# Performance work log

Hardware: AMD Instinct MI355X
Metric: run time of the kernel (lower is better)

The kernel has to match this reference:

```python
import jax, jax.numpy as jnp
import numpy as np

B, H, L = 16, 256, 4096
C, KD, NS = 1, 32, 8  # channels, kernel_dim, num_scales


def _interp_linear(k, s):
    """torch F.interpolate(mode='linear', align_corners=False) with integer scale s.
    k: (C, H, Lin) -> (C, H, Lin*s)."""
    if s == 1:
        return k
    Lin = k.shape[-1]
    x = (jnp.arange(Lin * s, dtype=jnp.float32) + 0.5) / s - 0.5
    x = jnp.clip(x, 0.0, Lin - 1)
    x0 = jnp.floor(x).astype(jnp.int32)
    x1 = jnp.minimum(x0 + 1, Lin - 1)
    w = (x - x0.astype(jnp.float32)).astype(k.dtype)
    return k[..., x0] * (1.0 - w) + k[..., x1] * w


def _build_kernel(kernels):
    # multiplier = linspace(decay_min=2, decay_max=2, H) -> all 2.0, shape (1,H,1)
    multiplier = jnp.linspace(2.0, 2.0, H).reshape(1, H, 1)
    parts = []
    for i in range(NS):
        s = 2 ** max(0, i - 1)  # init_scale = 0
        parts.append(_interp_linear(kernels[i], s) * multiplier ** (NS - i - 1))
    return jnp.concatenate(parts, axis=-1)  # (C, H, 4096)


def setup_inputs() -> dict:
    key = jax.random.key(0)
    k0, k1, k2, k3, k4 = jax.random.split(key, 5)
    u = jax.random.normal(k0, (B, H, L), jnp.float32)
    kernels = jax.random.normal(k1, (NS, C, H, KD), jnp.float32)
    D = jax.random.normal(k2, (C, H), jnp.float32)
    W_out = jax.random.normal(k3, (H, C * H), jnp.float32) * 0.05
    b_out = jax.random.normal(k4, (H,), jnp.float32) * 0.05
    return {"u": u, "kernels": kernels, "D": D, "W_out": W_out, "b_out": b_out}


def reference(u, kernels, D, W_out, b_out):
    k = _build_kernel(kernels)  # (C, H, Lk)
    Lk = k.shape[-1]
    if Lk > L:
        k = k[..., :L]
    elif Lk < L:
        k = jnp.pad(k, ((0, 0), (0, 0), (0, L - Lk)))
    # kernel_norm is detached on first forward
    norm = jax.lax.stop_gradient(jnp.linalg.norm(k, axis=-1, keepdims=True))
    k = k / norm
    n = 2 * L
    k_f = jnp.fft.rfft(k, n=n)  # (C, H, L+1) complex
    u_f = jnp.fft.rfft(u, n=n)  # (B, H, L+1) complex
    y_f = jnp.einsum('bhl,chl->bchl', u_f, k_f)
    y = jnp.fft.irfft(y_f, n=n)[..., :L]  # (B, C, H, L)
    y = y + jnp.einsum('bhl,ch->bchl', u, D)
    y = y.reshape(B, C * H, L)
    y = jax.nn.gelu(y, approximate=False)  # nn.GELU exact
    y = jnp.transpose(y, (0, 2, 1))  # (B, L, C*H)
    y = y @ W_out.T + b_out  # output_linear: C*H -> H
    return jnp.transpose(y, (0, 2, 1))  # (B, H, L)
```

## Files before the change

### kernel.cpp

```cpp
#include <hip/hip_runtime.h>


#define C1f 0.92387953251128674f
#define S1f 0.38268343236508977f
#define C2f 0.70710678118654752f

typedef __attribute__((ext_vector_type(8))) short bf16x8;
typedef __attribute__((ext_vector_type(4))) float f32x4;

static __device__ __forceinline__ unsigned short f2bf(float f) {
  unsigned u = __float_as_uint(f);
  u += 0x7FFFu + ((u >> 16) & 1u);
  return (unsigned short)(u >> 16);
}

static __device__ __forceinline__ void cmul(float& ar, float& ai, float br, float bi) {
  float t = ar * br - ai * bi;
  ai = ar * bi + ai * br;
  ar = t;
}

static __device__ __forceinline__ float gelu_t(float x) {
  float x2 = x * x;
  float t = x * __builtin_fmaf(0.044715f, x2, 1.f);
  float e = __builtin_amdgcn_exp2f(-2.3022650966f * t);
  return x * __builtin_amdgcn_rcpf(1.f + e);
}

#define LGKM()                                              \
  {                                                         \
    asm volatile("s_waitcnt lgkmcnt(0)" ::: "memory");      \
    __builtin_amdgcn_sched_barrier(0);                      \
  }

__device__ __constant__ float W32C[16] = {
  1.f, 0.98078528040323044913f, 0.92387953251128675613f, 0.83146961230254523708f,
  0.70710678118654752440f, 0.55557023301960222474f, 0.38268343236508977173f,
  0.19509032201612826785f, 0.f, -0.19509032201612826785f, -0.38268343236508977173f,
  -0.55557023301960222474f, -0.70710678118654752440f, -0.83146961230254523708f,
  -0.92387953251128675613f, -0.98078528040323044913f};
__device__ __constant__ float W32S[16] = {
  0.f, 0.19509032201612826785f, 0.38268343236508977173f, 0.55557023301960222474f,
  0.70710678118654752440f, 0.83146961230254523708f, 0.92387953251128675613f,
  0.98078528040323044913f, 1.f, 0.98078528040323044913f, 0.92387953251128675613f,
  0.83146961230254523708f, 0.70710678118654752440f, 0.55557023301960222474f,
  0.38268343236508977173f, 0.19509032201612826785f};

template <bool ZH>
static __device__ __forceinline__ void dft16_fwd_t(float* xr, float* xi) {
  const float wr[8] = {1.f, C1f, C2f, S1f, 0.f, -S1f, -C2f, -C1f};
  const float wi[8] = {0.f, -S1f, -C2f, -C1f, -1.f, -C1f, -C2f, -S1f};
#pragma unroll
  for (int j = 0; j < 8; ++j) {
    if (ZH) {
      float ar = xr[j], ai = xi[j];
      xr[j + 8] = ar * wr[j] - ai * wi[j];
      xi[j + 8] = ar * wi[j] + ai * wr[j];
    } else {
      float ar = xr[j], ai = xi[j], br = xr[j + 8], bi = xi[j + 8];
      xr[j] = ar + br; xi[j] = ai + bi;
      float dr = ar - br, di = ai - bi;
      xr[j + 8] = dr * wr[j] - di * wi[j];
      xi[j + 8] = dr * wi[j] + di * wr[j];
    }
  }
#pragma unroll
  for (int h = 0; h < 2; ++h) {
#pragma unroll
    for (int j = 0; j < 4; ++j) {
      int i0 = h * 8 + j, i1 = i0 + 4;
      float ar = xr[i0], ai = xi[i0], br = xr[i1], bi = xi[i1];
      xr[i0] = ar + br; xi[i0] = ai + bi;
      float dr = ar - br, di = ai - bi;
      xr[i1] = dr * wr[2 * j] - di * wi[2 * j];
      xi[i1] = dr * wi[2 * j] + di * wr[2 * j];
    }
  }
#pragma unroll
  for (int h = 0; h < 4; ++h) {
    int base = h * 4;
    {
      int i0 = base, i1 = base + 2;
      float ar = xr[i0], ai = xi[i0], br = xr[i1], bi = xi[i1];
      xr[i0] = ar + br; xi[i0] = ai + bi;
      xr[i1] = ar - br; xi[i1] = ai - bi;
    }
    {
      int i0 = base + 1, i1 = base + 3;
      float ar = xr[i0], ai = xi[i0], br = xr[i1], bi = xi[i1];
      xr[i0] = ar + br; xi[i0] = ai + bi;
      float dr = ar - br, di = ai - bi;
      xr[i1] = di; xi[i1] = -dr;
    }
  }
#pragma unroll
  for (int h = 0; h < 8; ++h) {
    int i0 = h * 2, i1 = i0 + 1;
    float ar = xr[i0], ai = xi[i0], br = xr[i1], bi = xi[i1];
    xr[i0] = ar + br; xi[i0] = ai + bi;
    xr[i1] = ar - br; xi[i1] = ai - bi;
  }
}

template <bool HALF>
static __device__ __forceinline__ void dft16_inv_t(float* xr, float* xi) {
  const float wr[8] = {1.f, C1f, C2f, S1f, 0.f, -S1f, -C2f, -C1f};
  const float wi[8] = {0.f, S1f, C2f, C1f, 1.f, C1f, C2f, S1f};
#pragma unroll
  for (int h = 0; h < 8; ++h) {
    int i0 = h * 2, i1 = i0 + 1;
    float ar = xr[i0], ai = xi[i0], br = xr[i1], bi = xi[i1];
    xr[i0] = ar + br; xi[i0] = ai + bi;
    xr[i1] = ar - br; xi[i1] = ai - bi;
  }
#pragma unroll
  for (int h = 0; h < 4; ++h) {
    int base = h * 4;
    {
      int i0 = base, i1 = base + 2;
      float ar = xr[i0], ai = xi[i0], tr = xr[i1], ti = xi[i1];
      xr[i0] = ar + tr; xi[i0] = ai + ti;
      xr[i1] = ar - tr; xi[i1] = ai - ti;
    }
    {
      int i0 = base + 1, i1 = base + 3;
      float ar = xr[i0], ai = xi[i0], br = xr[i1], bi = xi[i1];
      float tr = -bi, ti = br;
      xr[i0] = ar + tr; xi[i0] = ai + ti;
      xr[i1] = ar - tr; xi[i1] = ai - ti;
    }
  }
#pragma unroll
  for (int h = 0; h < 2; ++h) {
#pragma unroll
    for (int j = 0; j < 4; ++j) {
      int i0 = h * 8 + j, i1 = i0 + 4;
      float br = xr[i1], bi = xi[i1];
      float tr = br * wr[2 * j] - bi * wi[2 * j];
      float ti = br * wi[2 * j] + bi * wr[2 * j];
      float ar = xr[i0], ai = xi[i0];
      xr[i0] = ar + tr; xi[i0] = ai + ti;
      xr[i1] = ar - tr; xi[i1] = ai - ti;
    }
  }
#pragma unroll
  for (int j = 0; j < 8; ++j) {
    int i0 = j, i1 = j + 8;
    float br = xr[i1], bi = xi[i1];
    float tr = br * wr[j] - bi * wi[j];
    float ti = br * wi[j] + bi * wr[j];
    float ar = xr[i0], ai = xi[i0];
    xr[i0] = ar + tr; xi[i0] = ai + ti;
    if (!HALF) { xr[i1] = ar - tr; xi[i1] = ai - ti; }
  }
}

#define REV_INIT constexpr int REV[16] = {0, 8, 4, 12, 2, 10, 6, 14, 1, 9, 5, 13, 3, 11, 7, 15}

#define TWCHAIN(XR, XI, CR, CI)                         \
  {                                                     \
    float pr_ = (CR), pi_ = (CI);                       \
    cmul(XR[8], XI[8], pr_, pi_);                       \
    _Pragma("unroll") for (int k = 2; k < 16; ++k) {    \
      cmul(pr_, pi_, (CR), (CI));                       \
      cmul(XR[REV[k]], XI[REV[k]], pr_, pi_);           \
    }                                                   \
  }

static __device__ __forceinline__ void fft8192_fwd(float* xr, float* xi, float* lbuf,
                                                   int t, const float2* __restrict__ tw) {
  REV_INIT;
  int bs1 = t + (t >> 5);
  int bg1 = ((t >> 5) << 9) + (t & 31) + ((t >> 5) << 4);
  int qq = t & 1;
  int bg2 = 33 * (t >> 1) + qq;
  dft16_fwd_t<true>(xr, xi);
  {
    float2 w1 = tw[t];
    TWCHAIN(xr, xi, w1.x, w1.y);
  }
#pragma unroll
  for (int j = 0; j < 16; ++j) lbuf[bs1 + 528 * REV[j]] = xr[j];
  __syncthreads();
#pragma unroll
  for (int m = 0; m < 16; ++m) xr[m] = lbuf[bg1 + 33 * m];
  __syncthreads();
#pragma unroll
  for (int j = 0; j < 16; ++j) lbuf[bs1 + 528 * REV[j]] = xi[j];
  __syncthreads();
#pragma unroll
  for (int m = 0; m < 16; ++m) xi[m] = lbuf[bg1 + 33 * m];
  dft16_fwd_t<false>(xr, xi);
  {
    float2 w1 = tw[(t & 31) << 4];
    TWCHAIN(xr, xi, w1.x, w1.y);
  }
  LGKM();
#pragma unroll
  for (int j = 0; j < 16; ++j) lbuf[bg1 + 33 * REV[j]] = xr[j];
  LGKM();
#pragma unroll
  for (int m = 0; m < 16; ++m) xr[m] = lbuf[bg2 + 2 * m];
  LGKM();
#pragma unroll
  for (int j = 0; j < 16; ++j) lbuf[bg1 + 33 * REV[j]] = xi[j];
  LGKM();
#pragma unroll
  for (int m = 0; m < 16; ++m) xi[m] = lbuf[bg2 + 2 * m];
  dft16_fwd_t<false>(xr, xi);
  if (qq) {
#pragma unroll
    for (int k = 1; k < 16; ++k) cmul(xr[REV[k]], xi[REV[k]], W32C[k], -W32S[k]);
  }
  float sgn = qq ? -1.f : 1.f;
#pragma unroll
  for (int j = 0; j < 16; ++j) {
    float pr = __shfl_xor(xr[j], 1);
    float pi = __shfl_xor(xi[j], 1);
    xr[j] = sgn * xr[j] + pr;
    xi[j] = sgn * xi[j] + pi;
  }
}

static __device__ __forceinline__ void fft8192_inv(float* xr, float* xi, float* lbuf,
                                                   int t, const float2* __restrict__ tw) {
  REV_INIT;
  int bs1 = t + (t >> 5);
  int bg1 = ((t >> 5) << 9) + (t & 31) + ((t >> 5) << 4);
  int qq = t & 1;
  int bg2 = 33 * (t >> 1) + qq;
  float sgn = qq ? -1.f : 1.f;
#pragma unroll
  for (int j = 0; j < 16; ++j) {
    float pr = __shfl_xor(xr[j], 1);
    float pi = __shfl_xor(xi[j], 1);
    xr[j] = sgn * xr[j] + pr;
    xi[j] = sgn * xi[j] + pi;
  }
  if (qq) {
#pragma unroll
    for (int k = 1; k < 16; ++k) cmul(xr[REV[k]], xi[REV[k]], W32C[k], W32S[k]);
  }
  dft16_inv_t<false>(xr, xi);
  LGKM();
#pragma unroll
  for (int m = 0; m < 16; ++m) lbuf[bg2 + 2 * m] = xr[m];
  LGKM();
#pragma unroll
  for (int j = 0; j < 16; ++j) xr[j] = lbuf[bg1 + 33 * REV[j]];
  LGKM();
#pragma unroll
  for (int m = 0; m < 16; ++m) lbuf[bg2 + 2 * m] = xi[m];
  LGKM();
#pragma unroll
  for (int j = 0; j < 16; ++j) xi[j] = lbuf[bg1 + 33 * REV[j]];
  {
    float2 w1 = tw[(t & 31) << 4];
    TWCHAIN(xr, xi, w1.x, -w1.y);
  }
  dft16_inv_t<false>(xr, xi);
  LGKM();
#pragma unroll
  for (int m = 0; m < 16; ++m) lbuf[bg1 + 33 * m] = xr[m];
  __syncthreads();
#pragma unroll
  for (int j = 0; j < 16; ++j) xr[j] = lbuf[bs1 + 528 * REV[j]];
  __syncthreads();
#pragma unroll
  for (int m = 0; m < 16; ++m) lbuf[bg1 + 33 * m] = xi[m];
  __syncthreads();
#pragma unroll
  for (int j = 0; j < 16; ++j) xi[j] = lbuf[bs1 + 528 * REV[j]];
  {
    float2 w1 = tw[t];
    TWCHAIN(xr, xi, w1.x, -w1.y);
  }
  dft16_inv_t<true>(xr, xi);
}

__global__ void __launch_bounds__(256) gconv_setup(
    const float* __restrict__ kernels,
    const float* __restrict__ W_out,
    float* __restrict__ k_norm,
    float2* __restrict__ tw,
    unsigned short* __restrict__ Wbf)
{
  int blk = blockIdx.x;
  int tid = threadIdx.x;
  if (blk < 256) {
    int h = blk;
    __shared__ float red[256];
    float val[16];
    float ss = 0.0f;
#pragma unroll
    for (int r = 0; r < 16; ++r) {
      int l = tid + 256 * r;
      int i;
      if (l < 32) i = 0;
      else if (l < 64) i = 1;
      else i = (31 - __clz(l)) - 4;
      int off = (i == 0) ? 0 : (16 << i);
      int s = (i <= 1) ? 1 : (1 << (i - 1));
      float mult = (float)(1 << (7 - i));
      int j = l - off;
      const float* kb = kernels + ((size_t)i * 256 + h) * 32;
      float v;
      if (s == 1) {
        v = kb[j];
      } else {
        float x = ((float)j + 0.5f) / (float)s - 0.5f;
        x = fminf(fmaxf(x, 0.0f), 31.0f);
        float xf = floorf(x);
        int x0 = (int)xf;
        int x1 = min(x0 + 1, 31);
        float w = x - xf;
        v = kb[x0] * (1.0f - w) + kb[x1] * w;
      }
      v *= mult;
      val[r] = v;
      ss += v * v;
    }
    red[tid] = ss;
    __syncthreads();
    for (int o = 128; o > 0; o >>= 1) {
      if (tid < o) red[tid] += red[tid + o];
      __syncthreads();
    }
    float inv = 1.0f / sqrtf(red[0]);
#pragma unroll
    for (int r = 0; r < 16; ++r)
      k_norm[(size_t)h * 4096 + tid + 256 * r] = val[r] * inv;
  } else if (blk < 258) {
    int idx = (blk - 256) * 256 + tid;
    double ang = -6.283185307179586477 * (double)idx / 8192.0;
    tw[idx] = make_float2((float)cos(ang), (float)sin(ang));
  } else {
    int o = (blk - 258) * 256 + tid;
    Wbf[o] = f2bf(W_out[o]);
  }
}

__global__ void __launch_bounds__(512, 4) gconv_kfft(
    const float* __restrict__ k_norm,
    const float* __restrict__ Dvec,
    const float2* __restrict__ tw,
    float2* __restrict__ Kst)
{
  __shared__ float lbuf[8448];
  int h = blockIdx.x;
  int t = threadIdx.x;
  float xr[16], xi[16];
  const float* kn = k_norm + ((size_t)h << 12);
#pragma unroll
  for (int m = 0; m < 8; ++m) { xr[m] = kn[t + (m << 9)]; xi[m] = 0.f; }
#pragma unroll
  for (int m = 8; m < 16; ++m) { xr[m] = 0.f; xi[m] = 0.f; }
  fft8192_fwd(xr, xi, lbuf, t, tw);
  float Dh = Dvec[h];
  const float sc = 1.0f / 8192.0f;
  float2* out = Kst + ((size_t)h << 13) + (t << 4);
#pragma unroll
  for (int j = 0; j < 16; ++j)
    out[j] = make_float2((xr[j] + Dh) * sc, xi[j] * sc);
}

__global__ void __launch_bounds__(512, 4) gconv_main(
    const float* __restrict__ u,
    const float2* __restrict__ tw,
    const float2* __restrict__ Kst,
    unsigned short* __restrict__ g)
{
  __shared__ float lbuf[8448];
  int blk = blockIdx.x;
  int h = blk & 255;
  int pb = blk >> 8;
  int t = threadIdx.x;
  const float* u0 = u + ((size_t)(pb * 256 + h) << 12);
  const float* u1 = u + ((size_t)((pb + 8) * 256 + h) << 12);
  float xr[16], xi[16];
#pragma unroll
  for (int m = 0; m < 8; ++m) { xr[m] = u0[t + (m << 9)]; xi[m] = u1[t + (m << 9)]; }
#pragma unroll
  for (int m = 8; m < 16; ++m) { xr[m] = 0.f; xi[m] = 0.f; }
  fft8192_fwd(xr, xi, lbuf, t, tw);
  const float2* kr = Kst + ((size_t)h << 13) + (t << 4);
#pragma unroll
  for (int j = 0; j < 16; ++j) {
    float2 kv = kr[j];
    cmul(xr[j], xi[j], kv.x, kv.y);
  }
  fft8192_inv(xr, xi, lbuf, t, tw);
  unsigned short* g0 = g + ((size_t)(pb * 256 + h) << 12) + t;
  unsigned short* g1 = g + ((size_t)((pb + 8) * 256 + h) << 12) + t;
#pragma unroll
  for (int m = 0; m < 8; ++m) {
    g0[m << 9] = f2bf(gelu_t(xr[m]));
    g1[m << 9] = f2bf(gelu_t(xi[m]));
  }
}

__global__ void __launch_bounds__(256) gconv_out(
    const unsigned short* __restrict__ g,
    const unsigned short* __restrict__ Wbf,
    const float* __restrict__ b_out,
    float* __restrict__ out)
{
  __shared__ unsigned short As[128][40];
  __shared__ unsigned short Bs[32][132];
  int l0 = blockIdx.x * 128;
  int m0 = blockIdx.y * 128;
  int b  = blockIdx.z;
  int tid = threadIdx.x;
  int lane = tid & 63, wid = tid >> 6;
  int wm = (wid >> 1) * 64, wl = (wid & 1) * 64;
  int lhi = lane >> 4, llo = lane & 15;
  f32x4 acc[4][4];
#pragma unroll
  for (int a = 0; a < 4; ++a)
#pragma unroll
    for (int c = 0; c < 4; ++c) acc[a][c] = (f32x4){0.f, 0.f, 0.f, 0.f};

  for (int ks = 0; ks < 8; ++ks) {
    int k0 = ks * 32;
#pragma unroll
    for (int i = 0; i < 2; ++i) {
      int idx = tid + i * 256;
      int m = idx >> 2, c = idx & 3;
      *(uint4*)&As[m][c * 8] =
          *(const uint4*)(Wbf + ((size_t)(m0 + m) << 8) + k0 + c * 8);
      int k = idx >> 4, cc = idx & 15;
      const unsigned short* gp =
          g + ((size_t)(b * 256 + k0 + k) << 12) + l0 + cc * 8;
      ((uint2*)&Bs[k][cc * 8])[0] = ((const uint2*)gp)[0];
      ((uint2*)&Bs[k][cc * 8])[1] = ((const uint2*)gp)[1];
    }
    __syncthreads();
    int kk = lhi * 8;
    bf16x8 af[4], bfr[4];
#pragma unroll
    for (int f = 0; f < 4; ++f)
      af[f] = *(bf16x8*)&As[wm + f * 16 + llo][kk];
#pragma unroll
    for (int f = 0; f < 4; ++f) {
      bf16x8 v;
#pragma unroll
      for (int j = 0; j < 8; ++j)
        v[j] = (short)Bs[kk + j][wl + f * 16 + llo];
      bfr[f] = v;
    }
#pragma unroll
    for (int fm = 0; fm < 4; ++fm)
#pragma unroll
      for (int fl = 0; fl < 4; ++fl)
        acc[fm][fl] = __builtin_amdgcn_mfma_f32_16x16x32_bf16(
            af[fm], bfr[fl], acc[fm][fl], 0, 0, 0);
    __syncthreads();
  }
#pragma unroll
  for (int fm = 0; fm < 4; ++fm) {
#pragma unroll
    for (int r = 0; r < 4; ++r) {
      int m = m0 + wm + fm * 16 + lhi * 4 + r;
      float bias = b_out[m];
      float* op = out + ((size_t)(b * 256 + m) << 12) + l0 + wl + llo;
#pragma unroll
      for (int fl = 0; fl < 4; ++fl)
        op[fl * 16] = acc[fm][fl][r] + bias;
    }
  }
}

extern "C" void kernel_launch(void* const* d_in, const int* in_sizes, int n_in,
                              void* d_out, int out_size, void* d_ws, size_t ws_size,
                              hipStream_t stream) {
  (void)in_sizes; (void)n_in; (void)out_size; (void)ws_size;
  const float* u       = (const float*)d_in[0];
  const float* kernels = (const float*)d_in[1];
  const float* Dvec    = (const float*)d_in[2];
  const float* W_out   = (const float*)d_in[3];
  const float* b_out   = (const float*)d_in[4];
  float* out = (float*)d_out;
  char* ws = (char*)d_ws;

  float*  k_norm = (float*)(ws);
  float2* tw     = (float2*)(ws + (4u << 20));
  unsigned short* Wbf = (unsigned short*)(ws + (4u << 20) + (128u << 10));
  float2* Kst    = (float2*)(ws + (8u << 20));
  unsigned short* g = (unsigned short*)(ws + (24u << 20));

  gconv_setup<<<514, 256, 0, stream>>>(kernels, W_out, k_norm, tw, Wbf);
  gconv_kfft<<<256, 512, 0, stream>>>(k_norm, Dvec, tw, Kst);
  gconv_main<<<2048, 512, 0, stream>>>(u, tw, Kst, g);
  dim3 gd(32, 2, 16);
  gconv_out<<<gd, 256, 0, stream>>>(g, Wbf, b_out, out);
}
```

Measured before the change: 106.7 us.

## Process two batch-pairs per block with interleaved software-pipelined FFT stages

gconv_main now handles two complex FFT pairs (four batch rows) per block and interleaves their stages, so the register-level DFT work of one pair overlaps the shared-memory transposes and barriers of the other. The grid is halved to 1024 blocks. Twiddles and the kernel-spectrum pointer are loaded once and reused for both pairs. The cost is twice the register arrays per thread, which under launch bounds (512,4) risks spills or lower occupancy.

```diff
diff --git a/kernel.cpp b/kernel.cpp
--- a/kernel.cpp
+++ b/kernel.cpp
@@ -220,62 +220,6 @@
     xr[j] = sgn * xr[j] + pr;
     xi[j] = sgn * xi[j] + pi;
   }
-}
-
-static __device__ __forceinline__ void fft8192_inv(float* xr, float* xi, float* lbuf,
-                                                   int t, const float2* __restrict__ tw) {
-  REV_INIT;
-  int bs1 = t + (t >> 5);
-  int bg1 = ((t >> 5) << 9) + (t & 31) + ((t >> 5) << 4);
-  int qq = t & 1;
-  int bg2 = 33 * (t >> 1) + qq;
-  float sgn = qq ? -1.f : 1.f;
-#pragma unroll
-  for (int j = 0; j < 16; ++j) {
-    float pr = __shfl_xor(xr[j], 1);
-    float pi = __shfl_xor(xi[j], 1);
-    xr[j] = sgn * xr[j] + pr;
-    xi[j] = sgn * xi[j] + pi;
-  }
-  if (qq) {
-#pragma unroll
-    for (int k = 1; k < 16; ++k) cmul(xr[REV[k]], xi[REV[k]], W32C[k], W32S[k]);
-  }
-  dft16_inv_t<false>(xr, xi);
-  LGKM();
-#pragma unroll
-  for (int m = 0; m < 16; ++m) lbuf[bg2 + 2 * m] = xr[m];
-  LGKM();
-#pragma unroll
-  for (int j = 0; j < 16; ++j) xr[j] = lbuf[bg1 + 33 * REV[j]];
-  LGKM();
-#pragma unroll
-  for (int m = 0; m < 16; ++m) lbuf[bg2 + 2 * m] = xi[m];
-  LGKM();
-#pragma unroll
-  for (int j = 0; j < 16; ++j) xi[j] = lbuf[bg1 + 33 * REV[j]];
-  {
-    float2 w1 = tw[(t & 31) << 4];
-    TWCHAIN(xr, xi, w1.x, -w1.y);
-  }
-  dft16_inv_t<false>(xr, xi);
-  LGKM();
-#pragma unroll
-  for (int m = 0; m < 16; ++m) lbuf[bg1 + 33 * m] = xr[m];
-  __syncthreads();
-#pragma unroll
-  for (int j = 0; j < 16; ++j) xr[j] = lbuf[bs1 + 528 * REV[j]];
-  __syncthreads();
-#pragma unroll
-  for (int m = 0; m < 16; ++m) lbuf[bg1 + 33 * m] = xi[m];
-  __syncthreads();
-#pragma unroll
-  for (int j = 0; j < 16; ++j) xi[j] = lbuf[bs1 + 528 * REV[j]];
-  {
-    float2 w1 = tw[t];
-    TWCHAIN(xr, xi, w1.x, -w1.y);
-  }
-  dft16_inv_t<true>(xr, xi);
 }
 
 __global__ void __launch_bounds__(256) gconv_setup(
@@ -371,31 +315,140 @@
     unsigned short* __restrict__ g)
 {
   __shared__ float lbuf[8448];
+  REV_INIT;
   int blk = blockIdx.x;
   int h = blk & 255;
-  int pb = blk >> 8;
+  int pp = blk >> 8;
   int t = threadIdx.x;
-  const float* u0 = u + ((size_t)(pb * 256 + h) << 12);
-  const float* u1 = u + ((size_t)((pb + 8) * 256 + h) << 12);
-  float xr[16], xi[16];
-#pragma unroll
-  for (int m = 0; m < 8; ++m) { xr[m] = u0[t + (m << 9)]; xi[m] = u1[t + (m << 9)]; }
-#pragma unroll
-  for (int m = 8; m < 16; ++m) { xr[m] = 0.f; xi[m] = 0.f; }
-  fft8192_fwd(xr, xi, lbuf, t, tw);
+  int bs1 = t + (t >> 5);
+  int bg1 = ((t >> 5) << 9) + (t & 31) + ((t >> 5) << 4);
+  int qq = t & 1;
+  int bg2 = 33 * (t >> 1) + qq;
+  float sgn = qq ? -1.f : 1.f;
+  float2 w1t = tw[t];
+  float2 w2t = tw[(t & 31) << 4];
   const float2* kr = Kst + ((size_t)h << 13) + (t << 4);
-#pragma unroll
-  for (int j = 0; j < 16; ++j) {
-    float2 kv = kr[j];
-    cmul(xr[j], xi[j], kv.x, kv.y);
-  }
-  fft8192_inv(xr, xi, lbuf, t, tw);
-  unsigned short* g0 = g + ((size_t)(pb * 256 + h) << 12) + t;
-  unsigned short* g1 = g + ((size_t)((pb + 8) * 256 + h) << 12) + t;
-#pragma unroll
-  for (int m = 0; m < 8; ++m) {
-    g0[m << 9] = f2bf(gelu_t(xr[m]));
-    g1[m << 9] = f2bf(gelu_t(xi[m]));
+
+#define T1W(X) {_Pragma("unroll") for (int j = 0; j < 16; ++j) lbuf[bs1 + 528 * REV[j]] = X[j];}
+#define T1R(X) {_Pragma("unroll") for (int m = 0; m < 16; ++m) X[m] = lbuf[bg1 + 33 * m];}
+#define I2W(X) {_Pragma("unroll") for (int j = 0; j < 16; ++j) lbuf[bg1 + 33 * REV[j]] = X[j];}
+#define I2R(X) {_Pragma("unroll") for (int m = 0; m < 16; ++m) X[m] = lbuf[bg2 + 2 * m];}
+#define I3W(X) {_Pragma("unroll") for (int m = 0; m < 16; ++m) lbuf[bg2 + 2 * m] = X[m];}
+#define I3R(X) {_Pragma("unroll") for (int j = 0; j < 16; ++j) X[j] = lbuf[bg1 + 33 * REV[j]];}
+#define T4W(X) {_Pragma("unroll") for (int m = 0; m < 16; ++m) lbuf[bg1 + 33 * m] = X[m];}
+#define T4R(X) {_Pragma("unroll") for (int j = 0; j < 16; ++j) X[j] = lbuf[bs1 + 528 * REV[j]];}
+#define S4(XR, XI) {_Pragma("unroll") for (int j = 0; j < 16; ++j) { \
+    float pr = __shfl_xor(XR[j], 1); float pi = __shfl_xor(XI[j], 1); \
+    XR[j] = sgn * XR[j] + pr; XI[j] = sgn * XI[j] + pi; }}
+#define S3TWF(XR, XI) if (qq) {_Pragma("unroll") for (int k = 1; k < 16; ++k) \
+    cmul(XR[REV[k]], XI[REV[k]], W32C[k], -W32S[k]);}
+#define S3TWI(XR, XI) if (qq) {_Pragma("unroll") for (int k = 1; k < 16; ++k) \
+    cmul(XR[REV[k]], XI[REV[k]], W32C[k], W32S[k]);}
+#define MULTK(XR, XI) {_Pragma("unroll") for (int j = 0; j < 16; ++j) { \
+    float2 kv = kr[j]; cmul(XR[j], XI[j], kv.x, kv.y); }}
+
+  float xrA[16], xiA[16], xrB[16], xiB[16];
+  const float* uA0 = u + ((size_t)(pp * 256 + h) << 12);
+  const float* uA1 = u + ((size_t)((pp + 8) * 256 + h) << 12);
+  const float* uB0 = u + ((size_t)((pp + 4) * 256 + h) << 12);
+  const float* uB1 = u + ((size_t)((pp + 12) * 256 + h) << 12);
+#pragma unroll
+  for (int m = 0; m < 8; ++m) { xrA[m] = uA0[t + (m << 9)]; xiA[m] = uA1[t + (m << 9)]; }
+  dft16_fwd_t<true>(xrA, xiA);
+  TWCHAIN(xrA, xiA, w1t.x, w1t.y);
+  T1W(xrA);
+#pragma unroll
+  for (int m = 0; m < 8; ++m) { xrB[m] = uB0[t + (m << 9)]; xiB[m] = uB1[t + (m << 9)]; }
+  dft16_fwd_t<true>(xrB, xiB);
+  TWCHAIN(xrB, xiB, w1t.x, w1t.y);
+  __syncthreads();
+  T1R(xrA);
+  __syncthreads();
+  T1W(xiA);
+  __syncthreads();
+  T1R(xiA);
+  dft16_fwd_t<false>(xrA, xiA);
+  TWCHAIN(xrA, xiA, w2t.x, w2t.y);
+  LGKM(); I2W(xrA);
+  LGKM(); I2R(xrA);
+  LGKM(); I2W(xiA);
+  LGKM(); I2R(xiA);
+  __syncthreads();
+  T1W(xrB);
+  dft16_fwd_t<false>(xrA, xiA);
+  S3TWF(xrA, xiA);
+  S4(xrA, xiA);
+  MULTK(xrA, xiA);
+  S4(xrA, xiA);
+  S3TWI(xrA, xiA);
+  dft16_inv_t<false>(xrA, xiA);
+  __syncthreads();
+  T1R(xrB);
+  __syncthreads();
+  T1W(xiB);
+  __syncthreads();
+  T1R(xiB);
+  dft16_fwd_t<false>(xrB, xiB);
+  TWCHAIN(xrB, xiB, w2t.x, w2t.y);
+  LGKM(); I2W(xrB);
+  LGKM(); I2R(xrB);
+  LGKM(); I2W(xiB);
+  LGKM(); I2R(xiB);
+  LGKM(); I3W(xrA);
+  LGKM(); I3R(xrA);
+  LGKM(); I3W(xiA);
+  LGKM(); I3R(xiA);
+  TWCHAIN(xrA, xiA, w2t.x, -w2t.y);
+  dft16_inv_t<false>(xrA, xiA);
+  dft16_fwd_t<false>(xrB, xiB);
+  S3TWF(xrB, xiB);
+  S4(xrB, xiB);
+  MULTK(xrB, xiB);
+  S4(xrB, xiB);
+  S3TWI(xrB, xiB);
+  dft16_inv_t<false>(xrB, xiB);
+  LGKM(); T4W(xrA);
+  __syncthreads();
+  T4R(xrA);
+  __syncthreads();
+  T4W(xiA);
+  __syncthreads();
+  T4R(xiA);
+  TWCHAIN(xrA, xiA, w1t.x, -w1t.y);
+  dft16_inv_t<true>(xrA, xiA);
+  {
+    unsigned short* g0 = g + ((size_t)(pp * 256 + h) << 12) + t;
+    unsigned short* g1 = g + ((size_t)((pp + 8) * 256 + h) << 12) + t;
+#pragma unroll
+    for (int m = 0; m < 8; ++m) {
+      g0[m << 9] = f2bf(gelu_t(xrA[m]));
+      g1[m << 9] = f2bf(gelu_t(xiA[m]));
+    }
+  }
+  __syncthreads();
+  LGKM(); I3W(xrB);
+  LGKM(); I3R(xrB);
+  LGKM(); I3W(xiB);
+  LGKM(); I3R(xiB);
+  TWCHAIN(xrB, xiB, w2t.x, -w2t.y);
+  dft16_inv_t<false>(xrB, xiB);
+  LGKM(); T4W(xrB);
+  __syncthreads();
+  T4R(xrB);
+  __syncthreads();
+  T4W(xiB);
+  __syncthreads();
+  T4R(xiB);
+  TWCHAIN(xrB, xiB, w1t.x, -w1t.y);
+  dft16_inv_t<true>(xrB, xiB);
+  {
+    unsigned short* g0 = g + ((size_t)((pp + 4) * 256 + h) << 12) + t;
+    unsigned short* g1 = g + ((size_t)((pp + 12) * 256 + h) << 12) + t;
+#pragma unroll
+    for (int m = 0; m < 8; ++m) {
+      g0[m << 9] = f2bf(gelu_t(xrB[m]));
+      g1[m << 9] = f2bf(gelu_t(xiB[m]));
+    }
   }
 }
 
@@ -490,7 +543,7 @@
 
   gconv_setup<<<514, 256, 0, stream>>>(kernels, W_out, k_norm, tw, Wbf);
   gconv_kfft<<<256, 512, 0, stream>>>(k_norm, Dvec, tw, Kst);
-  gconv_main<<<2048, 512, 0, stream>>>(u, tw, Kst, g);
+  gconv_main<<<1024, 512, 0, stream>>>(u, tw, Kst, g);
   dim3 gd(32, 2, 16);
   gconv_out<<<gd, 256, 0, stream>>>(g, Wbf, b_out, out);
 }
```

After: 145.1 us. 1.36x slower.
